# Optimization experiments

Measured on AMD Instinct MI355X. Metric: run time of the kernel, lower is better.

## Reference

```python
import jax, jax.numpy as jnp
import numpy as np

D = 512
H = 8
DK = D // H
FF = 4 * D
EPS = 1e-5
NEG = -1.0e9


def _layernorm(x, g, b):
    mu = jnp.mean(x, axis=-1, keepdims=True)
    var = jnp.mean((x - mu) ** 2, axis=-1, keepdims=True)
    return (x - mu) * jax.lax.rsqrt(var + EPS) * g + b


def setup_inputs() -> dict:
    key = jax.random.key(0)
    ks = jax.random.split(key, 16)
    B, S = 4, 2048
    x = jax.random.normal(ks[0], (B, S, D), dtype=jnp.float32)
    # causal mask, broadcastable to [B, H, S, S]; mask==0 -> blocked
    mask = jnp.tril(jnp.ones((S, S), dtype=jnp.int32))[None, None]
    s = 1.0 / np.sqrt(D)
    sf = 1.0 / np.sqrt(FF)
    p = {
        "wq": jax.random.normal(ks[1], (D, D), jnp.float32) * s,
        "bq": jnp.zeros((D,), jnp.float32),
        "wk": jax.random.normal(ks[2], (D, D), jnp.float32) * s,
        "bk": jnp.zeros((D,), jnp.float32),
        "wv": jax.random.normal(ks[3], (D, D), jnp.float32) * s,
        "bv": jnp.zeros((D,), jnp.float32),
        "wo": jax.random.normal(ks[4], (D, D), jnp.float32) * s,
        "bo": jnp.zeros((D,), jnp.float32),
        "w1": jax.random.normal(ks[5], (D, FF), jnp.float32) * s,
        "b1": jnp.zeros((FF,), jnp.float32),
        "w2": jax.random.normal(ks[6], (FF, D), jnp.float32) * sf,
        "b2": jnp.zeros((D,), jnp.float32),
        "g1": jnp.ones((D,), jnp.float32),
        "be1": jnp.zeros((D,), jnp.float32),
        "g2": jnp.ones((D,), jnp.float32),
        "be2": jnp.zeros((D,), jnp.float32),
    }
    return {"x": x, "mask": mask, **p}


def reference(x, mask, wq, bq, wk, bk, wv, bv, wo, bo, w1, b1, w2, b2, g1, be1, g2, be2):
    B, S, _ = x.shape
    # projections -> [B, H, S, DK]
    q = (x @ wq + bq).reshape(B, S, H, DK).transpose(0, 2, 1, 3)
    k = (x @ wk + bk).reshape(B, S, H, DK).transpose(0, 2, 1, 3)
    v = (x @ wv + bv).reshape(B, S, H, DK).transpose(0, 2, 1, 3)
    scores = jnp.einsum("bhqd,bhkd->bhqk", q, k) / np.sqrt(DK)
    scores = jnp.where(mask == 0, NEG, scores)
    attn = jax.nn.softmax(scores, axis=-1)
    ctx = jnp.einsum("bhqk,bhkd->bhqd", attn, v)
    ctx = ctx.transpose(0, 2, 1, 3).reshape(B, S, D)
    attn_out = ctx @ wo + bo
    # dropout is inference-mode identity
    h = _layernorm(x + attn_out, g1, be1)
    ffn = jax.nn.relu(h @ w1 + b1) @ w2 + b2
    return _layernorm(h + ffn, g2, be2)
```

## Files before the change

kernel.cpp:

```cpp
#include <hip/hip_runtime.h>
#include <math.h>

#define D_   512
#define H_   8
#define DK_  64
#define FF_  2048
#define S_   2048
#define B_   4
#define M_   (B_*S_)
#define EPS_ 1e-5f
#define SCLQ 0.1803368801111f

typedef __attribute__((ext_vector_type(8))) short bf16x8;
typedef __attribute__((ext_vector_type(4))) float f32x4;
typedef __attribute__((ext_vector_type(4))) unsigned int u32x4;

__device__ inline unsigned short f2b(float f) {
    unsigned u = __builtin_bit_cast(unsigned, f);
    unsigned r = (u + 0x7FFFu + ((u >> 16) & 1u)) >> 16;
    return (unsigned short)r;
}
__device__ inline float b2f(unsigned short u) {
    return __builtin_bit_cast(float, (unsigned)u << 16);
}
__device__ inline unsigned packbf(float p0, float p1) {
    unsigned r;
    asm("v_cvt_pk_bf16_f32 %0, %1, %2" : "=v"(r) : "v"(p0), "v"(p1));
    return r;
}

__device__ __forceinline__ void async_cp16(const void* g, void* l) {
    __builtin_amdgcn_global_load_lds(
        (const __attribute__((address_space(1))) unsigned int*)g,
        (__attribute__((address_space(3))) unsigned int*)l, 16, 0, 0);
}

__global__ __launch_bounds__(256)
void prep_kernel(const float* __restrict__ x,
                 const float* __restrict__ wq, const float* __restrict__ wk,
                 const float* __restrict__ wv, const float* __restrict__ wo,
                 const float* __restrict__ bq, const float* __restrict__ bk,
                 const float* __restrict__ bv,
                 const float* __restrict__ w1, const float* __restrict__ w2,
                 unsigned short* __restrict__ xb, unsigned short* __restrict__ wqkvt,
                 unsigned short* __restrict__ wot, unsigned short* __restrict__ w1t,
                 unsigned short* __restrict__ w2t, float* __restrict__ bqkv)
{
    __shared__ float L[32][33];
    const int bid = blockIdx.x;
    const int tid = threadIdx.x;

    if (bid < 2048) {
        const int i = (bid * 256 + tid) * 8;
        const float4 a = *(const float4*)(x + i);
        const float4 b = *(const float4*)(x + i + 4);
        bf16x8 v;
        v[0] = (short)f2b(a.x); v[1] = (short)f2b(a.y);
        v[2] = (short)f2b(a.z); v[3] = (short)f2b(a.w);
        v[4] = (short)f2b(b.x); v[5] = (short)f2b(b.y);
        v[6] = (short)f2b(b.z); v[7] = (short)f2b(b.w);
        *(bf16x8*)(xb + i) = v;
        return;
    }

    const float* w; unsigned short* wt; int K, N, k0, n0; float scl = 1.f;
    if (bid < 3072) {
        const int z = (bid - 2048) >> 8;
        const int r = (bid - 2048) & 255;
        n0 = (r & 15) * 32; k0 = (r >> 4) * 32; K = 512; N = 512;
        w  = (z == 0) ? wq : (z == 1) ? wk : (z == 2) ? wv : wo;
        wt = (z < 3) ? (wqkvt + (size_t)z * 512 * 512) : wot;
        if (z == 0) scl = SCLQ;
        if (z < 3 && r == 0) {
            const float* bsrc = (z == 0) ? bq : (z == 1) ? bk : bv;
            const float bscl  = (z == 0) ? SCLQ : 1.f;
            bqkv[z * 512 + tid]       = bsrc[tid] * bscl;
            bqkv[z * 512 + 256 + tid] = bsrc[256 + tid] * bscl;
        }
    } else if (bid < 4096) {
        const int r = bid - 3072;
        n0 = (r & 63) * 32; k0 = (r >> 6) * 32; K = 512; N = 2048;
        w = w1; wt = w1t;
    } else {
        const int r = bid - 4096;
        n0 = (r & 15) * 32; k0 = (r >> 4) * 32; K = 2048; N = 512;
        w = w2; wt = w2t;
    }

    const int xx = tid & 31, y = tid >> 5;
#pragma unroll
    for (int i = 0; i < 4; i++)
        L[y + i * 8][xx] = w[(size_t)(k0 + y + i * 8) * N + n0 + xx] * scl;
    __syncthreads();
#pragma unroll
    for (int i = 0; i < 4; i++)
        wt[(size_t)(n0 + y + i * 8) * K + k0 + xx] = f2b(L[xx][y + i * 8]);
}

template<int WR, int WC, int MT, int NT, int BK, int OUTB, int RELU, int RESADD, int HASBIAS>
__global__ __launch_bounds__(256)
void gemm_bf16(const unsigned short* __restrict__ A, const unsigned short* __restrict__ Bt,
               const float* __restrict__ bias, const void* __restrict__ RES,
               void* __restrict__ Cv, int K, int lda, int ldb, int ldc)
{
    constexpr int BM  = WR * MT * 16;
    constexpr int BN  = WC * NT * 16;
    constexpr int CPR = BK / 8;
    constexpr int CA  = BM * BK / (256 * 8);
    constexpr int CB  = BN * BK / (256 * 8);
    __shared__ unsigned short As[2][BM * BK];
    __shared__ unsigned short Bs[2][BN * BK];

    const int tid  = threadIdx.x;
    const int lane = tid & 63;
    const int w    = tid >> 6;
    const int wr   = w / WC, wc = w % WC;
    const int quad = lane >> 4;
    const int l15  = lane & 15;
    const int n0   = blockIdx.x * BN;
    const int m0   = blockIdx.y * BM;

    f32x4 acc[MT][NT];
#pragma unroll
    for (int i = 0; i < MT; i++)
#pragma unroll
        for (int j = 0; j < NT; j++) acc[i][j] = (f32x4){0.f, 0.f, 0.f, 0.f};

    auto stage = [&](int k0, int bufi) {
#pragma unroll
        for (int i = 0; i < CA; i++) {
            const int c   = tid + i * 256;
            const int row = c / CPR;
            int l = c % CPR;
            if (BK == 64) l ^= (row & 7);
            async_cp16(&A[(size_t)(m0 + row) * lda + k0 + l * 8], &As[bufi][c * 8]);
        }
#pragma unroll
        for (int i = 0; i < CB; i++) {
            const int c   = tid + i * 256;
            const int row = c / CPR;
            int l = c % CPR;
            if (BK == 64) l ^= (row & 7);
            async_cp16(&Bt[(size_t)(n0 + row) * ldb + k0 + l * 8], &Bs[bufi][c * 8]);
        }
    };

    stage(0, 0);
    const int niter = K / BK;
    for (int ii = 0; ii < niter; ii++) {
        const int knext = (ii + 1 < niter) ? (ii + 1) * BK : 0;
        stage(knext, (ii + 1) & 1);
        __builtin_amdgcn_s_waitcnt(0x0f70 | (CA + CB));
        __builtin_amdgcn_s_barrier();

        const unsigned short* Ac = &As[ii & 1][0];
        const unsigned short* Bc = &Bs[ii & 1][0];
#pragma unroll
        for (int ks = 0; ks < BK / 32; ks++) {
            bf16x8 af[MT], bfr[NT];
#pragma unroll
            for (int t = 0; t < MT; t++) {
                const int r = wr * MT * 16 + t * 16 + l15;
                int ch = (ks << 2) | quad;
                if (BK == 64) ch ^= (r & 7);
                af[t] = *(const bf16x8*)&Ac[r * BK + ch * 8];
            }
#pragma unroll
            for (int t = 0; t < NT; t++) {
                const int r = wc * NT * 16 + t * 16 + l15;
                int ch = (ks << 2) | quad;
                if (BK == 64) ch ^= (r & 7);
                bfr[t] = *(const bf16x8*)&Bc[r * BK + ch * 8];
            }
#pragma unroll
            for (int mt = 0; mt < MT; mt++)
#pragma unroll
                for (int nt = 0; nt < NT; nt++)
                    acc[mt][nt] = __builtin_amdgcn_mfma_f32_16x16x32_bf16(
                        af[mt], bfr[nt], acc[mt][nt], 0, 0, 0);
        }
        __builtin_amdgcn_s_barrier();
    }

#pragma unroll
    for (int mt = 0; mt < MT; mt++) {
        const int rowb = m0 + wr * MT * 16 + mt * 16 + quad * 4;
#pragma unroll
        for (int nt = 0; nt < NT; nt++) {
            const int col = n0 + wc * NT * 16 + nt * 16 + l15;
            const float bv = HASBIAS ? bias[col] : 0.f;
#pragma unroll
            for (int r = 0; r < 4; r++) {
                const size_t idx = (size_t)(rowb + r) * ldc + col;
                float v = acc[mt][nt][r] + bv;
                if (RESADD == 1) v += ((const float*)RES)[idx];
                if (RESADD == 2) v += b2f(((const unsigned short*)RES)[idx]);
                if (RELU)   v = fmaxf(v, 0.f);
                if (OUTB) ((unsigned short*)Cv)[idx] = f2b(v);
                else      ((float*)Cv)[idx] = v;
            }
        }
    }
}

__global__ __launch_bounds__(256)
void vtrans(const unsigned short* __restrict__ qkv, unsigned short* __restrict__ vt)
{
    __shared__ unsigned short L[64][72];
    const int s0 = blockIdx.x * 64;
    const int bh = blockIdx.y;
    const int b  = bh >> 3, hh = bh & 7;
    const int tid = threadIdx.x;
    const unsigned short* src = qkv + (size_t)(b * S_) * 1536 + 1024 + hh * 64;
#pragma unroll
    for (int i = 0; i < 2; i++) {
        const int c = tid + i * 256;
        const int r = c >> 3, sub = (c & 7) * 8;
        *(bf16x8*)&L[r][sub] = *(const bf16x8*)(src + (size_t)(s0 + r) * 1536 + sub);
    }
    __syncthreads();
    const int dk = tid >> 2;
    const int sc = (tid & 3) * 16;
    bf16x8 t0, t1;
#pragma unroll
    for (int j = 0; j < 8; j++) t0[j] = (short)L[sc + j][dk];
#pragma unroll
    for (int j = 0; j < 8; j++) t1[j] = (short)L[sc + 8 + j][dk];
    unsigned short* dst = vt + (size_t)(bh * 64 + dk) * S_ + s0 + sc;
    *(bf16x8*)(dst)     = t0;
    *(bf16x8*)(dst + 8) = t1;
}

__global__ __launch_bounds__(256, 4)
void attn_mfma(const unsigned short* __restrict__ qkv,
               const unsigned short* __restrict__ vt,
               unsigned short* __restrict__ ctx)
{
    __shared__ unsigned short Arena[20480];

    const int tid  = threadIdx.x;
    const int lane = tid & 63;
    const int w    = tid >> 6;
    const int quad = lane >> 4;
    const int l15  = lane & 15;
    const int bid  = blockIdx.x;
    const int g    = bid >> 5;
    const int qb   = (g < 8) ? 31 - g : (g < 16) ? g + 8 : (g < 24) ? 31 - g : g - 24;
    const int bh   = bid & 31;
    const int b    = bh >> 3, hh = bh & 7;
    const int kh   = w & 1;
    const int qh   = w >> 1;

    const unsigned short* qbase = qkv + (size_t)(b * S_) * 1536 + hh * 64;
    const unsigned short* kbase = qbase + 512;
    const unsigned short* vtb   = vt + (size_t)bh * 64 * S_;
    unsigned short* Pb = &Arena[16384];

    bf16x8 ones;
#pragma unroll
    for (int j = 0; j < 8; j++) ones[j] = (short)0x3F80;

    auto stage = [&](int kb, int bufi) {
        unsigned short* kd = &Arena[bufi * 4096];
        unsigned short* vd = &Arena[8192 + bufi * 4096];
#pragma unroll
        for (int i = 0; i < 2; i++) {
            const int c = tid + i * 256;
            const int row = c >> 3;
            const int l = (c & 7) ^ (row & 7);
            async_cp16(kbase + (size_t)(kb * 64 + row) * 1536 + l * 8, kd + c * 8);
            async_cp16(vtb + (size_t)row * S_ + kb * 64 + l * 8, vd + c * 8);
        }
    };

    bf16x8 qf[2][2];
#pragma unroll
    for (int qt = 0; qt < 2; qt++) {
        const unsigned short* qr = qbase + (size_t)(qb * 64 + qh * 32 + qt * 16 + l15) * 1536;
        qf[qt][0] = *(const bf16x8*)(qr + quad * 8);
        qf[qt][1] = *(const bf16x8*)(qr + 32 + quad * 8);
    }

    f32x4 Oacc[2][5];
#pragma unroll
    for (int qt = 0; qt < 2; qt++)
#pragma unroll
        for (int i = 0; i < 5; i++) Oacc[qt][i] = (f32x4){0.f, 0.f, 0.f, 0.f};

    stage(0, 0);

    const int physv = (kh * 4 + quad) ^ (l15 & 7);
    const int sw    = (l15 & 7) << 3;

    for (int kb = 0; kb < qb; kb++) {
        stage(kb + 1, (kb + 1) & 1);
        __builtin_amdgcn_s_waitcnt(0x0F74);
        __builtin_amdgcn_s_barrier();
        const unsigned short* Kc = &Arena[(kb & 1) * 4096];
        const unsigned short* Vc = &Arena[8192 + (kb & 1) * 4096];

        f32x4 st[2][2];
#pragma unroll
        for (int qt = 0; qt < 2; qt++)
#pragma unroll
            for (int kt = 0; kt < 2; kt++) st[qt][kt] = (f32x4){0.f, 0.f, 0.f, 0.f};
#pragma unroll
        for (int kc = 0; kc < 2; kc++) {
            const int phys = (kc * 4 + quad) ^ (l15 & 7);
            const bf16x8 kf0 = *(const bf16x8*)&Kc[(kh * 32 + l15) * 64 + phys * 8];
            const bf16x8 kf1 = *(const bf16x8*)&Kc[(kh * 32 + 16 + l15) * 64 + phys * 8];
#pragma unroll
            for (int qt = 0; qt < 2; qt++) {
                st[qt][0] = __builtin_amdgcn_mfma_f32_16x16x32_bf16(kf0, qf[qt][kc], st[qt][0], 0, 0, 0);
                st[qt][1] = __builtin_amdgcn_mfma_f32_16x16x32_bf16(kf1, qf[qt][kc], st[qt][1], 0, 0, 0);
            }
        }

        bf16x8 vf[4];
#pragma unroll
        for (int nt = 0; nt < 4; nt++)
            vf[nt] = *(const bf16x8*)&Vc[(nt * 16 + l15) * 64 + physv * 8];

#pragma unroll
        for (int qt = 0; qt < 2; qt++) {
            const int qrow = qh * 32 + qt * 16 + l15;
#pragma unroll
            for (int kt = 0; kt < 2; kt++) {
                uint2 pw;
                pw.x = packbf(exp2f(st[qt][kt][0]), exp2f(st[qt][kt][1]));
                pw.y = packbf(exp2f(st[qt][kt][2]), exp2f(st[qt][kt][3]));
                *(uint2*)&Pb[qrow * 64 + ((kh * 32 + kt * 16 + quad * 4) ^ sw)] = pw;
            }
        }
        asm volatile("s_waitcnt lgkmcnt(0)" ::: "memory");

#pragma unroll
        for (int qt = 0; qt < 2; qt++) {
            const int qrow = qh * 32 + qt * 16 + l15;
            const bf16x8 af = *(const bf16x8*)&Pb[qrow * 64 + ((kh * 32 + quad * 8) ^ sw)];
#pragma unroll
            for (int nt = 0; nt < 4; nt++)
                Oacc[qt][nt] = __builtin_amdgcn_mfma_f32_16x16x32_bf16(af, vf[nt], Oacc[qt][nt], 0, 0, 0);
            Oacc[qt][4] = __builtin_amdgcn_mfma_f32_16x16x32_bf16(af, ones, Oacc[qt][4], 0, 0, 0);
        }
        __builtin_amdgcn_s_barrier();
    }

    {
        stage(0, (qb + 1) & 1);
        __builtin_amdgcn_s_waitcnt(0x0F74);
        __builtin_amdgcn_s_barrier();
        const unsigned short* Kc = &Arena[(qb & 1) * 4096];
        const unsigned short* Vc = &Arena[8192 + (qb & 1) * 4096];

        const bool skipDiag = (kh == 1 && qh == 0);
        const bool fullDiag = (kh == 0 && qh == 1);

        if (!skipDiag) {
            f32x4 st[2][2];
#pragma unroll
            for (int qt = 0; qt < 2; qt++)
#pragma unroll
                for (int kt = 0; kt < 2; kt++) st[qt][kt] = (f32x4){0.f, 0.f, 0.f, 0.f};
#pragma unroll
            for (int kc = 0; kc < 2; kc++) {
                const int phys = (kc * 4 + quad) ^ (l15 & 7);
                const bf16x8 kf0 = *(const bf16x8*)&Kc[(kh * 32 + l15) * 64 + phys * 8];
                const bf16x8 kf1 = *(const bf16x8*)&Kc[(kh * 32 + 16 + l15) * 64 + phys * 8];
#pragma unroll
                for (int qt = 0; qt < 2; qt++) {
                    st[qt][0] = __builtin_amdgcn_mfma_f32_16x16x32_bf16(kf0, qf[qt][kc], st[qt][0], 0, 0, 0);
                    st[qt][1] = __builtin_amdgcn_mfma_f32_16x16x32_bf16(kf1, qf[qt][kc], st[qt][1], 0, 0, 0);
                }
            }

            uint2 pw[2][2];
            if (fullDiag) {
#pragma unroll
                for (int qt = 0; qt < 2; qt++)
#pragma unroll
                    for (int kt = 0; kt < 2; kt++) {
                        pw[qt][kt].x = packbf(exp2f(st[qt][kt][0]), exp2f(st[qt][kt][1]));
                        pw[qt][kt].y = packbf(exp2f(st[qt][kt][2]), exp2f(st[qt][kt][3]));
                    }
            } else {
                float p[4];
#pragma unroll
                for (int r = 0; r < 4; r++)
                    p[r] = (quad * 4 + r > l15) ? 0.f : exp2f(st[0][0][r]);
                pw[0][0].x = packbf(p[0], p[1]);
                pw[0][0].y = packbf(p[2], p[3]);
                pw[0][1].x = 0u; pw[0][1].y = 0u;
                pw[1][0].x = packbf(exp2f(st[1][0][0]), exp2f(st[1][0][1]));
                pw[1][0].y = packbf(exp2f(st[1][0][2]), exp2f(st[1][0][3]));
#pragma unroll
                for (int r = 0; r < 4; r++)
                    p[r] = (quad * 4 + r > l15) ? 0.f : exp2f(st[1][1][r]);
                pw[1][1].x = packbf(p[0], p[1]);
                pw[1][1].y = packbf(p[2], p[3]);
            }

            bf16x8 vf[4];
#pragma unroll
            for (int nt = 0; nt < 4; nt++)
                vf[nt] = *(const bf16x8*)&Vc[(nt * 16 + l15) * 64 + physv * 8];

#pragma unroll
            for (int qt = 0; qt < 2; qt++) {
                const int qrow = qh * 32 + qt * 16 + l15;
#pragma unroll
                for (int kt = 0; kt < 2; kt++)
                    *(uint2*)&Pb[qrow * 64 + ((kh * 32 + kt * 16 + quad * 4) ^ sw)] = pw[qt][kt];
            }
            asm volatile("s_waitcnt lgkmcnt(0)" ::: "memory");
#pragma unroll
            for (int qt = 0; qt < 2; qt++) {
                const int qrow = qh * 32 + qt * 16 + l15;
                const bf16x8 af = *(const bf16x8*)&Pb[qrow * 64 + ((kh * 32 + quad * 8) ^ sw)];
#pragma unroll
                for (int nt = 0; nt < 4; nt++)
                    Oacc[qt][nt] = __builtin_amdgcn_mfma_f32_16x16x32_bf16(af, vf[nt], Oacc[qt][nt], 0, 0, 0);
                Oacc[qt][4] = __builtin_amdgcn_mfma_f32_16x16x32_bf16(af, ones, Oacc[qt][4], 0, 0, 0);
            }
        }
    }

    __syncthreads();
    float* red = (float*)&Arena[0];
    const int rbase = (qh * 64 + lane) * 44;
    if (kh) {
#pragma unroll
        for (int qt = 0; qt < 2; qt++)
#pragma unroll
            for (int i = 0; i < 5; i++)
                *(f32x4*)&red[rbase + (qt * 5 + i) * 4] = Oacc[qt][i];
    }
    __syncthreads();
    if (!kh) {
#pragma unroll
        for (int qt = 0; qt < 2; qt++)
#pragma unroll
            for (int i = 0; i < 5; i++)
                Oacc[qt][i] += *(const f32x4*)&red[rbase + (qt * 5 + i) * 4];

        unsigned short* cb = ctx + (size_t)(b * S_) * 512 + hh * 64;
#pragma unroll
        for (int qt = 0; qt < 2; qt++) {
            const int orow = qb * 64 + qh * 32 + qt * 16 + quad * 4;
#pragma unroll
            for (int r = 0; r < 4; r++) {
                const float inv = 1.f / Oacc[qt][4][r];
#pragma unroll
                for (int nt = 0; nt < 4; nt++)
                    cb[(size_t)(orow + r) * 512 + nt * 16 + l15] = f2b(Oacc[qt][nt][r] * inv);
            }
        }
    }
}

template<int WF, int WB>
__global__ __launch_bounds__(256)
void ln_kernel(const float* __restrict__ s, const float* __restrict__ g,
               const float* __restrict__ be, float* __restrict__ out,
               unsigned short* __restrict__ outb)
{
    const int wave = threadIdx.x >> 6;
    const int lane = threadIdx.x & 63;
    const int row  = blockIdx.x * 4 + wave;
    const float* ps = s + (size_t)row * D_;
    const int c0 = lane * 4;

    float v[8];
    {
        const float4 a0 = *(const float4*)(ps + c0);
        const float4 a1 = *(const float4*)(ps + c0 + 256);
        v[0] = a0.x; v[1] = a0.y; v[2] = a0.z; v[3] = a0.w;
        v[4] = a1.x; v[5] = a1.y; v[6] = a1.z; v[7] = a1.w;
    }

    float sum = 0.f;
#pragma unroll
    for (int i = 0; i < 8; i++) sum += v[i];
#pragma unroll
    for (int m = 1; m < 64; m <<= 1) sum += __shfl_xor(sum, m);
    const float mu = sum * (1.f / D_);

    float sq = 0.f;
#pragma unroll
    for (int i = 0; i < 8; i++) { const float d = v[i] - mu; sq += d * d; }
#pragma unroll
    for (int m = 1; m < 64; m <<= 1) sq += __shfl_xor(sq, m);
    const float rstd = rsqrtf(sq * (1.f / D_) + EPS_);

    const float4 g0 = *(const float4*)(g + c0);
    const float4 b0 = *(const float4*)(be + c0);
    const float4 g1 = *(const float4*)(g + c0 + 256);
    const float4 b1 = *(const float4*)(be + c0 + 256);

    float o[8];
    o[0] = (v[0] - mu) * rstd * g0.x + b0.x;
    o[1] = (v[1] - mu) * rstd * g0.y + b0.y;
    o[2] = (v[2] - mu) * rstd * g0.z + b0.z;
    o[3] = (v[3] - mu) * rstd * g0.w + b0.w;
    o[4] = (v[4] - mu) * rstd * g1.x + b1.x;
    o[5] = (v[5] - mu) * rstd * g1.y + b1.y;
    o[6] = (v[6] - mu) * rstd * g1.z + b1.z;
    o[7] = (v[7] - mu) * rstd * g1.w + b1.w;

    if (WF) {
        *(float4*)(out + (size_t)row * D_ + c0)       = *(float4*)&o[0];
        *(float4*)(out + (size_t)row * D_ + c0 + 256) = *(float4*)&o[4];
    }
    if (WB) {
        short4 vb0 = (short4){(short)f2b(o[0]), (short)f2b(o[1]), (short)f2b(o[2]), (short)f2b(o[3])};
        short4 vb1 = (short4){(short)f2b(o[4]), (short)f2b(o[5]), (short)f2b(o[6]), (short)f2b(o[7])};
        *(short4*)(outb + (size_t)row * D_ + c0)       = vb0;
        *(short4*)(outb + (size_t)row * D_ + c0 + 256) = vb1;
    }
}

extern "C" void kernel_launch(void* const* d_in, const int* in_sizes, int n_in,
                              void* d_out, int out_size, void* d_ws, size_t ws_size,
                              hipStream_t stream)
{
    const float* x  = (const float*)d_in[0];
    const float* wq = (const float*)d_in[2];
    const float* bq = (const float*)d_in[3];
    const float* wk = (const float*)d_in[4];
    const float* bk = (const float*)d_in[5];
    const float* wv = (const float*)d_in[6];
    const float* bv = (const float*)d_in[7];
    const float* wo = (const float*)d_in[8];
    const float* bo = (const float*)d_in[9];
    const float* w1 = (const float*)d_in[10];
    const float* b1 = (const float*)d_in[11];
    const float* w2 = (const float*)d_in[12];
    const float* b2 = (const float*)d_in[13];
    const float* g1 = (const float*)d_in[14];
    const float* be1= (const float*)d_in[15];
    const float* g2 = (const float*)d_in[16];
    const float* be2= (const float*)d_in[17];
    float* out = (float*)d_out;

    const size_t MB = 1048576;
    char* w8 = (char*)d_ws;
    unsigned short* wqkvt = (unsigned short*)(w8 + 0);
    unsigned short* wot   = (unsigned short*)(w8 + 1572864);
    unsigned short* w1t   = (unsigned short*)(w8 + 2097152);
    unsigned short* w2t   = (unsigned short*)(w8 + 4194304);
    float*          bqkv  = (float*)(w8 + 6291456);
    unsigned short* qkv   = (unsigned short*)(w8 + 8 * MB);
    unsigned short* ffn1b = qkv;
    unsigned short* xb    = (unsigned short*)(w8 + 40 * MB);
    unsigned short* ctx   = xb;
    unsigned short* vt    = (unsigned short*)(w8 + 48 * MB);
    unsigned short* hb    = vt;
    float*          pre   = (float*)(w8 + 56 * MB);

    const dim3 blk(256);

    prep_kernel<<<dim3(5120), blk, 0, stream>>>(
        x, wq, wk, wv, wo, bq, bk, bv, w1, w2, xb, wqkvt, wot, w1t, w2t, bqkv);

    gemm_bf16<2,2,4,4,32,1,0,0,1><<<dim3(12, 64), blk, 0, stream>>>(
        xb, wqkvt, bqkv, nullptr, qkv, 512, 512, 512, 1536);

    vtrans<<<dim3(32, 32), blk, 0, stream>>>(qkv, vt);

    attn_mfma<<<dim3(1024), blk, 0, stream>>>(qkv, vt, ctx);

    gemm_bf16<2,2,2,4,64,0,0,1,1><<<dim3(4, 128), blk, 0, stream>>>(
        ctx, wot, bo, x, pre, 512, 512, 512, 512);

    ln_kernel<1,1><<<dim3(M_ / 4), blk, 0, stream>>>(pre, g1, be1, pre, hb);

    gemm_bf16<2,2,4,4,32,1,1,0,1><<<dim3(16, 64), blk, 0, stream>>>(
        hb, w1t, b1, nullptr, ffn1b, 512, 512, 512, 2048);

    gemm_bf16<2,2,2,4,64,0,0,1,1><<<dim3(4, 128), blk, 0, stream>>>(
        ffn1b, w2t, b2, pre, pre, 2048, 2048, 2048, 512);

    ln_kernel<1,0><<<dim3(M_ / 4), blk, 0, stream>>>(pre, g2, be2, out, nullptr);
}
```

Before: 267.2 us.

## Feed softmax probabilities to PV MFMA directly from registers using 16x16x16 bf16

```diff
diff --git a/kernel.cpp b/kernel.cpp
--- a/kernel.cpp
+++ b/kernel.cpp
@@ -12,6 +12,7 @@
 #define SCLQ 0.1803368801111f
 
 typedef __attribute__((ext_vector_type(8))) short bf16x8;
+typedef __attribute__((ext_vector_type(4))) short bf16x4;
 typedef __attribute__((ext_vector_type(4))) float f32x4;
 typedef __attribute__((ext_vector_type(4))) unsigned int u32x4;
 
@@ -236,7 +237,7 @@
                const unsigned short* __restrict__ vt,
                unsigned short* __restrict__ ctx)
 {
-    __shared__ unsigned short Arena[20480];
+    __shared__ unsigned short Arena[16384];
 
     const int tid  = threadIdx.x;
     const int lane = tid & 63;
@@ -254,11 +255,10 @@
     const unsigned short* qbase = qkv + (size_t)(b * S_) * 1536 + hh * 64;
     const unsigned short* kbase = qbase + 512;
     const unsigned short* vtb   = vt + (size_t)bh * 64 * S_;
-    unsigned short* Pb = &Arena[16384];
-
-    bf16x8 ones;
-#pragma unroll
-    for (int j = 0; j < 8; j++) ones[j] = (short)0x3F80;
+
+    bf16x4 ones4;
+#pragma unroll
+    for (int j = 0; j < 4; j++) ones4[j] = (short)0x3F80;
 
     auto stage = [&](int kb, int bufi) {
         unsigned short* kd = &Arena[bufi * 4096];
@@ -289,8 +289,8 @@
 
     stage(0, 0);
 
-    const int physv = (kh * 4 + quad) ^ (l15 & 7);
-    const int sw    = (l15 & 7) << 3;
+    const int vch0 = (kh * 4 + (quad >> 1));
+    const int vsub = (quad & 1) * 4;
 
     for (int kb = 0; kb < qb; kb++) {
         stage(kb + 1, (kb + 1) & 1);
@@ -316,32 +316,29 @@
             }
         }
 
-        bf16x8 vf[4];
-#pragma unroll
-        for (int nt = 0; nt < 4; nt++)
-            vf[nt] = *(const bf16x8*)&Vc[(nt * 16 + l15) * 64 + physv * 8];
+        bf16x4 vf[2][4];
+#pragma unroll
+        for (int kt = 0; kt < 2; kt++)
+#pragma unroll
+            for (int nt = 0; nt < 4; nt++)
+                vf[kt][nt] = *(const bf16x4*)&Vc[(nt * 16 + l15) * 64 +
+                    (((vch0 + kt * 2) ^ (l15 & 7)) << 3) + vsub];
 
 #pragma unroll
         for (int qt = 0; qt < 2; qt++) {
-            const int qrow = qh * 32 + qt * 16 + l15;
 #pragma unroll
             for (int kt = 0; kt < 2; kt++) {
-                uint2 pw;
-                pw.x = packbf(exp2f(st[qt][kt][0]), exp2f(st[qt][kt][1]));
-                pw.y = packbf(exp2f(st[qt][kt][2]), exp2f(st[qt][kt][3]));
-                *(uint2*)&Pb[qrow * 64 + ((kh * 32 + kt * 16 + quad * 4) ^ sw)] = pw;
-            }
-        }
-        asm volatile("s_waitcnt lgkmcnt(0)" ::: "memory");
-
-#pragma unroll
-        for (int qt = 0; qt < 2; qt++) {
-            const int qrow = qh * 32 + qt * 16 + l15;
-            const bf16x8 af = *(const bf16x8*)&Pb[qrow * 64 + ((kh * 32 + quad * 8) ^ sw)];
-#pragma unroll
-            for (int nt = 0; nt < 4; nt++)
-                Oacc[qt][nt] = __builtin_amdgcn_mfma_f32_16x16x32_bf16(af, vf[nt], Oacc[qt][nt], 0, 0, 0);
-            Oacc[qt][4] = __builtin_amdgcn_mfma_f32_16x16x32_bf16(af, ones, Oacc[qt][4], 0, 0, 0);
+                uint2 aw;
+                aw.x = packbf(exp2f(st[qt][kt][0]), exp2f(st[qt][kt][1]));
+                aw.y = packbf(exp2f(st[qt][kt][2]), exp2f(st[qt][kt][3]));
+                const bf16x4 af = __builtin_bit_cast(bf16x4, aw);
+#pragma unroll
+                for (int nt = 0; nt < 4; nt++)
+                    Oacc[qt][nt] = __builtin_amdgcn_mfma_f32_16x16x16bf16_1k(
+                        af, vf[kt][nt], Oacc[qt][nt], 0, 0, 0);
+                Oacc[qt][4] = __builtin_amdgcn_mfma_f32_16x16x16bf16_1k(
+                    af, ones4, Oacc[qt][4], 0, 0, 0);
+            }
         }
         __builtin_amdgcn_s_barrier();
     }
@@ -374,54 +371,55 @@
                 }
             }
 
-            uint2 pw[2][2];
+            bf16x4 af[2][2];
             if (fullDiag) {
 #pragma unroll
                 for (int qt = 0; qt < 2; qt++)
 #pragma unroll
                     for (int kt = 0; kt < 2; kt++) {
-                        pw[qt][kt].x = packbf(exp2f(st[qt][kt][0]), exp2f(st[qt][kt][1]));
-                        pw[qt][kt].y = packbf(exp2f(st[qt][kt][2]), exp2f(st[qt][kt][3]));
+                        uint2 aw;
+                        aw.x = packbf(exp2f(st[qt][kt][0]), exp2f(st[qt][kt][1]));
+                        aw.y = packbf(exp2f(st[qt][kt][2]), exp2f(st[qt][kt][3]));
+                        af[qt][kt] = __builtin_bit_cast(bf16x4, aw);
                     }
             } else {
                 float p[4];
+                uint2 aw;
 #pragma unroll
                 for (int r = 0; r < 4; r++)
                     p[r] = (quad * 4 + r > l15) ? 0.f : exp2f(st[0][0][r]);
-                pw[0][0].x = packbf(p[0], p[1]);
-                pw[0][0].y = packbf(p[2], p[3]);
-                pw[0][1].x = 0u; pw[0][1].y = 0u;
-                pw[1][0].x = packbf(exp2f(st[1][0][0]), exp2f(st[1][0][1]));
-                pw[1][0].y = packbf(exp2f(st[1][0][2]), exp2f(st[1][0][3]));
+                aw.x = packbf(p[0], p[1]); aw.y = packbf(p[2], p[3]);
+                af[0][0] = __builtin_bit_cast(bf16x4, aw);
+                af[0][1] = (bf16x4){0, 0, 0, 0};
+                aw.x = packbf(exp2f(st[1][0][0]), exp2f(st[1][0][1]));
+                aw.y = packbf(exp2f(st[1][0][2]), exp2f(st[1][0][3]));
+                af[1][0] = __builtin_bit_cast(bf16x4, aw);
 #pragma unroll
                 for (int r = 0; r < 4; r++)
                     p[r] = (quad * 4 + r > l15) ? 0.f : exp2f(st[1][1][r]);
-                pw[1][1].x = packbf(p[0], p[1]);
-                pw[1][1].y = packbf(p[2], p[3]);
-            }
-
-            bf16x8 vf[4];
-#pragma unroll
-            for (int nt = 0; nt < 4; nt++)
-                vf[nt] = *(const bf16x8*)&Vc[(nt * 16 + l15) * 64 + physv * 8];
-
-#pragma unroll
-            for (int qt = 0; qt < 2; qt++) {
-                const int qrow = qh * 32 + qt * 16 + l15;
-#pragma unroll
-                for (int kt = 0; kt < 2; kt++)
-                    *(uint2*)&Pb[qrow * 64 + ((kh * 32 + kt * 16 + quad * 4) ^ sw)] = pw[qt][kt];
-            }
-            asm volatile("s_waitcnt lgkmcnt(0)" ::: "memory");
-#pragma unroll
-            for (int qt = 0; qt < 2; qt++) {
-                const int qrow = qh * 32 + qt * 16 + l15;
-                const bf16x8 af = *(const bf16x8*)&Pb[qrow * 64 + ((kh * 32 + quad * 8) ^ sw)];
+                aw.x = packbf(p[0], p[1]); aw.y = packbf(p[2], p[3]);
+                af[1][1] = __builtin_bit_cast(bf16x4, aw);
+            }
+
+            bf16x4 vf[2][4];
+#pragma unroll
+            for (int kt = 0; kt < 2; kt++)
 #pragma unroll
                 for (int nt = 0; nt < 4; nt++)
-                    Oacc[qt][nt] = __builtin_amdgcn_mfma_f32_16x16x32_bf16(af, vf[nt], Oacc[qt][nt], 0, 0, 0);
-                Oacc[qt][4] = __builtin_amdgcn_mfma_f32_16x16x32_bf16(af, ones, Oacc[qt][4], 0, 0, 0);
-            }
+                    vf[kt][nt] = *(const bf16x4*)&Vc[(nt * 16 + l15) * 64 +
+                        (((vch0 + kt * 2) ^ (l15 & 7)) << 3) + vsub];
+
+#pragma unroll
+            for (int qt = 0; qt < 2; qt++)
+#pragma unroll
+                for (int kt = 0; kt < 2; kt++) {
+#pragma unroll
+                    for (int nt = 0; nt < 4; nt++)
+                        Oacc[qt][nt] = __builtin_amdgcn_mfma_f32_16x16x16bf16_1k(
+                            af[qt][kt], vf[kt][nt], Oacc[qt][nt], 0, 0, 0);
+                    Oacc[qt][4] = __builtin_amdgcn_mfma_f32_16x16x16bf16_1k(
+                        af[qt][kt], ones4, Oacc[qt][4], 0, 0, 0);
+                }
         }
     }
 
```

Measured after the change: 268.8 us. No clear change (+0.6%).
